# Kernel tuning notes

Measured on AMD Instinct MI355X. Metric: run time of the kernel, lower is better.

Reference implementation:

```python
import jax, jax.numpy as jnp
import numpy as np

HIDDEN = 4096
N_HEADS = 32
N_KV = 32
HEAD_DIM = 128
T = 2048
EPS = 1e-5
ROPE_THETA = 1000000.0


def rms_norm(x, w, eps=EPS):
    var = jnp.mean(x * x, axis=-1, keepdims=True)
    return x * jax.lax.rsqrt(var + eps) * w


def apply_rope(x, positions):
    # x: [T, H, D] ; neox-style (rotate halves), full rotary_dim = HEAD_DIM
    half = HEAD_DIM // 2
    inv_freq = 1.0 / (ROPE_THETA ** (jnp.arange(0, half, dtype=jnp.float32) / half))
    ang = positions.astype(jnp.float32)[:, None] * inv_freq  # [T, half]
    cos = jnp.cos(ang)[:, None, :]  # [T, 1, half]
    sin = jnp.sin(ang)[:, None, :]
    x1, x2 = x[..., :half], x[..., half:]
    return jnp.concatenate([x1 * cos - x2 * sin, x2 * cos + x1 * sin], axis=-1)


def setup_inputs() -> dict:
    key = jax.random.key(0)
    ks = jax.random.split(key, 5)
    s = 0.02
    qkv_out = (N_HEADS + 2 * N_KV) * HEAD_DIM
    return {
        "hidden_states": jax.random.normal(ks[0], (T, HIDDEN), jnp.float32),
        "positions": jnp.arange(T, dtype=jnp.int32),
        "w_qkv": jax.random.normal(ks[1], (qkv_out, HIDDEN), jnp.float32) * s,
        "b_qkv": jax.random.normal(ks[2], (qkv_out,), jnp.float32) * s,
        "q_norm_w": jnp.ones((N_HEADS * HEAD_DIM,), jnp.float32),
        "k_norm_w": jnp.ones((N_KV * HEAD_DIM,), jnp.float32),
        "w_o": jax.random.normal(ks[3], (HIDDEN, N_HEADS * HEAD_DIM), jnp.float32) * s,
    }


def reference(hidden_states, positions, w_qkv, b_qkv, q_norm_w, k_norm_w, w_o):
    q_size = N_HEADS * HEAD_DIM
    kv_size = N_KV * HEAD_DIM
    qkv = hidden_states @ w_qkv.T + b_qkv  # [T, q+2kv]
    q, k, v = jnp.split(qkv, [q_size, q_size + kv_size], axis=-1)
    # QK RMSNorm over the full flattened q / k widths (as in Molmo)
    q = rms_norm(q, q_norm_w)
    k = rms_norm(k, k_norm_w)
    q = apply_rope(q.reshape(T, N_HEADS, HEAD_DIM), positions)
    k = apply_rope(k.reshape(T, N_KV, HEAD_DIM), positions)
    v = v.reshape(T, N_KV, HEAD_DIM)
    scale = HEAD_DIM ** -0.5
    scores = jnp.einsum("qhd,khd->hqk", q, k) * scale  # [H, T, T]
    causal = positions[:, None] >= positions[None, :]
    scores = jnp.where(causal[None], scores, jnp.float32(-1e30))
    probs = jax.nn.softmax(scores, axis=-1)
    attn = jnp.einsum("hqk,khd->qhd", probs, v).reshape(T, N_HEADS * HEAD_DIM)
    return attn @ w_o.T
```

## Files before the change

kernel.cpp:

```cpp
#include <hip/hip_runtime.h>
#include <hip/hip_bf16.h>

#define T_SEQ 2048
#define NH 32
#define HD 128
#define QKV_N 12288
#define V_OFF 8192

typedef __bf16 bf16;
typedef __attribute__((ext_vector_type(8))) __bf16 bf16x8;
typedef __attribute__((ext_vector_type(4))) float f32x4;

#define GLDS16(g, l)                                                        \
  __builtin_amdgcn_global_load_lds(                                         \
      (const __attribute__((address_space(1))) void*)(g),                   \
      (__attribute__((address_space(3))) void*)(l), 16, 0, 0)

__device__ inline bf16x8 load8(const bf16* p) { return *(const bf16x8*)p; }
__device__ inline bf16x8 load8(const float* p) {
    f32x4 a = *(const f32x4*)p;
    f32x4 b = *(const f32x4*)(p + 4);
    bf16x8 r;
    r[0] = (bf16)a[0]; r[1] = (bf16)a[1]; r[2] = (bf16)a[2]; r[3] = (bf16)a[3];
    r[4] = (bf16)b[0]; r[5] = (bf16)b[1]; r[6] = (bf16)b[2]; r[7] = (bf16)b[3];
    return r;
}

__global__ __launch_bounds__(256)
void f32_to_bf16(const float* __restrict__ in, bf16* __restrict__ out, int n8)
{
    for (int i = blockIdx.x * 256 + threadIdx.x; i < n8; i += gridDim.x * 256)
        *(bf16x8*)(out + (size_t)i * 8) = load8(in + (size_t)i * 8);
}

#define BM 128
#define BN 128
#define BK 32

template <typename TO>
__global__ __launch_bounds__(256, 2)
void gemm_bt_glds(const bf16* __restrict__ A, int lda,
                  const bf16* __restrict__ B,
                  const float* __restrict__ bias,
                  TO* __restrict__ C, int ldc,
                  int mTiles, int colPerXcd, int K)
{
    __shared__ bf16 sA[BM * BK];
    __shared__ bf16 sB[BN * BK];
    const int tid  = threadIdx.x;
    const int wave = tid >> 6, lane = tid & 63;
    const int quad = lane >> 4, l16 = lane & 15;
    const int wm = wave >> 1, wn = wave & 1;

    int b = blockIdx.x;
    int xcd = b & 7, i = b >> 3;
    const int rowBase = (i % mTiles) * BM;
    const int colBase = (xcd * colPerXcd + i / mTiles) * BN;

    f32x4 acc[4][4] = {};

    for (int k0 = 0; k0 < K; k0 += BK) {
        __syncthreads();
        for (int r = 0; r < 2; ++r) {
            int cb = wave * 128 + r * 64;
            int c  = cb + lane;
            int row = c >> 2, kg = c & 3;
            GLDS16(A + (size_t)(rowBase + row) * lda + k0 + kg * 8, sA + cb * 8);
            GLDS16(B + (size_t)(colBase + row) * K + k0 + kg * 8, sB + cb * 8);
        }
        __syncthreads();

        bf16x8 af[4], bfr[4];
        for (int mi = 0; mi < 4; ++mi)
            af[mi] = *(const bf16x8*)(sA + (wm * 64 + mi * 16 + l16) * BK + quad * 8);
        for (int ni = 0; ni < 4; ++ni)
            bfr[ni] = *(const bf16x8*)(sB + (wn * 64 + ni * 16 + l16) * BK + quad * 8);
        for (int mi = 0; mi < 4; ++mi)
            for (int ni = 0; ni < 4; ++ni)
                acc[mi][ni] = __builtin_amdgcn_mfma_f32_16x16x32_bf16(
                    af[mi], bfr[ni], acc[mi][ni], 0, 0, 0);
    }

    for (int ni = 0; ni < 4; ++ni) {
        int col = colBase + wn * 64 + ni * 16 + l16;
        float bv = bias ? bias[col] : 0.0f;
        for (int mi = 0; mi < 4; ++mi) {
            int row0 = rowBase + wm * 64 + mi * 16 + quad * 4;
            for (int r = 0; r < 4; ++r)
                C[(size_t)(row0 + r) * ldc + col] = (TO)(acc[mi][ni][r] + bv);
        }
    }
}

template <typename TA, typename TB, typename TO>
__global__ __launch_bounds__(256, 2)
void gemm_bt_bias(const TA* __restrict__ A, int lda,
                  const TB* __restrict__ B,
                  const float* __restrict__ bias,
                  TO* __restrict__ C, int ldc,
                  int M, int N, int K)
{
    __shared__ bf16 sA[BM * BK];
    __shared__ bf16 sB[BN * BK];
    const int tid  = threadIdx.x;
    const int wave = tid >> 6, lane = tid & 63;
    const int quad = lane >> 4, l16 = lane & 15;
    const int wm = wave >> 1, wn = wave & 1;
    const int rowBase = blockIdx.x * BM;
    const int colBase = blockIdx.y * BN;

    int c0 = wave * 128 + lane;
    int rowA0 = c0 >> 2, kgA0 = c0 & 3;
    int rowA1 = (c0 + 64) >> 2, kgA1 = (c0 + 64) & 3;

    f32x4 acc[4][4] = {};

    for (int k0 = 0; k0 < K; k0 += BK) {
        bf16x8 ra0 = load8(A + (size_t)(rowBase + rowA0) * lda + k0 + kgA0 * 8);
        bf16x8 ra1 = load8(A + (size_t)(rowBase + rowA1) * lda + k0 + kgA1 * 8);
        bf16x8 rb0 = load8(B + (size_t)(colBase + rowA0) * K + k0 + kgA0 * 8);
        bf16x8 rb1 = load8(B + (size_t)(colBase + rowA1) * K + k0 + kgA1 * 8);
        __syncthreads();
        *(bf16x8*)(sA + rowA0 * BK + kgA0 * 8) = ra0;
        *(bf16x8*)(sA + rowA1 * BK + kgA1 * 8) = ra1;
        *(bf16x8*)(sB + rowA0 * BK + kgA0 * 8) = rb0;
        *(bf16x8*)(sB + rowA1 * BK + kgA1 * 8) = rb1;
        __syncthreads();

        bf16x8 af[4], bfr[4];
        for (int mi = 0; mi < 4; ++mi)
            af[mi] = *(const bf16x8*)(sA + (wm * 64 + mi * 16 + l16) * BK + quad * 8);
        for (int ni = 0; ni < 4; ++ni)
            bfr[ni] = *(const bf16x8*)(sB + (wn * 64 + ni * 16 + l16) * BK + quad * 8);
        for (int mi = 0; mi < 4; ++mi)
            for (int ni = 0; ni < 4; ++ni)
                acc[mi][ni] = __builtin_amdgcn_mfma_f32_16x16x32_bf16(
                    af[mi], bfr[ni], acc[mi][ni], 0, 0, 0);
    }

    for (int ni = 0; ni < 4; ++ni) {
        int col = colBase + wn * 64 + ni * 16 + l16;
        float bv = bias ? bias[col] : 0.0f;
        for (int mi = 0; mi < 4; ++mi) {
            int row0 = rowBase + wm * 64 + mi * 16 + quad * 4;
            for (int r = 0; r < 4; ++r)
                C[(size_t)(row0 + r) * ldc + col] = (TO)(acc[mi][ni][r] + bv);
        }
    }
}

__global__ __launch_bounds__(256)
void rmsnorm_rope(bf16* __restrict__ qkv, const float* __restrict__ qw,
                  const float* __restrict__ kw, const int* __restrict__ pos)
{
    const int t   = blockIdx.x;
    const int sel = blockIdx.y;
    bf16* x = qkv + (size_t)t * QKV_N + sel * 4096;
    const float* w = sel ? kw : qw;
    const int tid = threadIdx.x;

    float ss = 0.f;
    {
        int i0 = tid * 16;
        bf16x8 a = *(const bf16x8*)(x + i0);
        bf16x8 b = *(const bf16x8*)(x + i0 + 8);
        for (int j = 0; j < 8; ++j) { float fa = (float)a[j]; ss += fa * fa; }
        for (int j = 0; j < 8; ++j) { float fb = (float)b[j]; ss += fb * fb; }
    }
    for (int off = 1; off < 64; off <<= 1) ss += __shfl_xor(ss, off, 64);
    __shared__ float red[4];
    if ((tid & 63) == 0) red[tid >> 6] = ss;
    __syncthreads();
    float tot = red[0] + red[1] + red[2] + red[3];
    float rstd = rsqrtf(tot * (1.0f / 4096.0f) + 1e-5f);

    float fp = (float)pos[t];
    for (int i = tid; i < 2048; i += 256) {
        int h = i >> 6;
        int d = i & 63;
        int base = h * 128 + d;
        float x1 = (float)x[base]      * rstd * w[base];
        float x2 = (float)x[base + 64] * rstd * w[base + 64];
        float ang = fp * exp2f(-(float)d * 0.31143075889569023f);
        float s, c;
        sincosf(ang, &s, &c);
        x[base]      = (bf16)(x1 * c - x2 * s);
        x[base + 64] = (bf16)(x2 * c + x1 * s);
    }
}

__global__ __launch_bounds__(256)
void v_transpose(const bf16* __restrict__ qkv, bf16* __restrict__ vt)
{
    __shared__ bf16 tile[64][65];
    int t0 = blockIdx.x * 64, d0 = blockIdx.y * 64, h = blockIdx.z;
    int x = threadIdx.x & 63, y4 = threadIdx.x >> 6;
    for (int yy = y4; yy < 64; yy += 4)
        tile[yy][x] = qkv[(size_t)(t0 + yy) * QKV_N + V_OFF + h * HD + d0 + x];
    __syncthreads();
    for (int yy = y4; yy < 64; yy += 4)
        vt[(size_t)(h * HD + d0 + yy) * T_SEQ + t0 + x] = tile[x][yy];
}

#define SKP 136
#define SVP 72
#define PBP 72

__global__ __launch_bounds__(256, 2)
void flash_attn(bf16* qkv, const bf16* vt)
{
    __shared__ bf16 sK[64 * SKP];
    __shared__ bf16 sV[128 * SVP];
    __shared__ bf16 pbuf[4 * 16 * PBP];

    const int tid  = threadIdx.x;
    const int wave = tid >> 6, lane = tid & 63;
    const int quad = lane >> 4, l16 = lane & 15;
    const int h    = blockIdx.y;
    const int blk  = blockIdx.x;
    const int q0w  = blk * 64 + wave * 16;

    bf16x8 qf[4];
    {
        const bf16* qrow = qkv + (size_t)(q0w + l16) * QKV_N + h * HD;
        for (int c = 0; c < 4; ++c)
            qf[c] = *(const bf16x8*)(qrow + c * 32 + quad * 8);
    }

    f32x4 oacc[8] = {};
    float m2[4], l[4];
    for (int r = 0; r < 4; ++r) { m2[r] = -1e30f; l[r] = 0.f; }

    const float sc = 0.08838834764831845f * 1.4426950408889634f;
    bf16* pb = pbuf + wave * 16 * PBP;
    const int rowa = q0w + quad * 4;
    const int kend = blk * 64;

    for (int kb = 0; kb <= kend; kb += 64) {
        __syncthreads();
        for (int j = 0; j < 4; ++j) {
            int c = tid + j * 256;
            int r = c >> 4, off = (c & 15) * 8;
            bf16x8 v = *(const bf16x8*)(qkv + (size_t)(kb + r) * QKV_N + 4096 + h * HD + off);
            *(bf16x8*)(sK + r * SKP + off) = v;
        }
        for (int j = 0; j < 4; ++j) {
            int c = tid + j * 256;
            int d = c >> 3, off = (c & 7) * 8;
            bf16x8 v = *(const bf16x8*)(vt + (size_t)(h * HD + d) * T_SEQ + kb + off);
            *(bf16x8*)(sV + d * SVP + off) = v;
        }
        __syncthreads();

        const bool diag = (kb == kend);
        const int stmax = diag ? (wave + 1) : 4;

        f32x4 s[4] = {};
        for (int st = 0; st < 4; ++st) {
            if (st >= stmax) break;
            const bf16* kbase = sK + (st * 16 + l16) * SKP + quad * 8;
            for (int c = 0; c < 4; ++c) {
                bf16x8 kf = *(const bf16x8*)(kbase + c * 32);
                s[st] = __builtin_amdgcn_mfma_f32_16x16x32_bf16(qf[c], kf, s[st], 0, 0, 0);
            }
        }
        for (int st = 0; st < 4; ++st) {
            int col = kb + st * 16 + l16;
            for (int r = 0; r < 4; ++r) {
                float v = s[st][r] * sc;
                s[st][r] = (col <= rowa + r) ? v : -1e30f;
            }
        }
        float alpha[4];
        for (int r = 0; r < 4; ++r) {
            float mx = fmaxf(fmaxf(s[0][r], s[1][r]), fmaxf(s[2][r], s[3][r]));
            for (int off = 1; off < 16; off <<= 1)
                mx = fmaxf(mx, __shfl_xor(mx, off, 64));
            float mnew = fmaxf(m2[r], mx);
            alpha[r] = exp2f(m2[r] - mnew);
            float ps = 0.f;
            for (int st = 0; st < 4; ++st) {
                float p = exp2f(s[st][r] - mnew);
                s[st][r] = p;
                ps += p;
            }
            for (int off = 1; off < 16; off <<= 1)
                ps += __shfl_xor(ps, off, 64);
            l[r] = l[r] * alpha[r] + ps;
            m2[r] = mnew;
        }
        for (int c = 0; c < 8; ++c)
            for (int r = 0; r < 4; ++r)
                oacc[c][r] *= alpha[r];
        for (int st = 0; st < 4; ++st)
            for (int r = 0; r < 4; ++r)
                pb[(quad * 4 + r) * PBP + st * 16 + l16] = (bf16)s[st][r];
        __builtin_amdgcn_s_waitcnt(0xC07F);
        for (int ph = 0; ph < 2; ++ph) {
            bf16x8 pf = *(const bf16x8*)(pb + l16 * PBP + ph * 32 + quad * 8);
            for (int c = 0; c < 8; ++c) {
                bf16x8 vf = *(const bf16x8*)(sV + (c * 16 + l16) * SVP + ph * 32 + quad * 8);
                oacc[c] = __builtin_amdgcn_mfma_f32_16x16x32_bf16(pf, vf, oacc[c], 0, 0, 0);
            }
        }
    }

    for (int r = 0; r < 4; ++r) {
        float inv = 1.0f / l[r];
        int t = q0w + quad * 4 + r;
        for (int c = 0; c < 8; ++c)
            qkv[(size_t)t * QKV_N + V_OFF + h * HD + c * 16 + l16] =
                (bf16)(oacc[c][r] * inv);
    }
}

extern "C" void kernel_launch(void* const* d_in, const int* in_sizes, int n_in,
                              void* d_out, int out_size, void* d_ws, size_t ws_size,
                              hipStream_t stream)
{
    const float* hidden   = (const float*)d_in[0];
    const int*   pos      = (const int*)d_in[1];
    const float* w_qkv    = (const float*)d_in[2];
    const float* b_qkv    = (const float*)d_in[3];
    const float* q_norm_w = (const float*)d_in[4];
    const float* k_norm_w = (const float*)d_in[5];
    const float* w_o      = (const float*)d_in[6];
    float* out = (float*)d_out;

    bf16* qkv = (bf16*)d_ws;
    bf16* vt  = qkv + (size_t)T_SEQ * QKV_N;
    bf16* wqb = vt  + (size_t)4096 * T_SEQ;
    bf16* wob = wqb + (size_t)QKV_N * 4096;
    bf16* hib = wob + (size_t)4096 * 4096;
    const size_t need = ((size_t)T_SEQ * QKV_N + (size_t)4096 * T_SEQ +
                         (size_t)QKV_N * 4096 + (size_t)4096 * 4096 +
                         (size_t)T_SEQ * 4096) * 2;

    if (ws_size >= need) {
        f32_to_bf16<<<2048, 256, 0, stream>>>(hidden, hib, T_SEQ * 4096 / 8);
        f32_to_bf16<<<8192, 256, 0, stream>>>(w_qkv, wqb, QKV_N * 4096 / 8);
        f32_to_bf16<<<4096, 256, 0, stream>>>(w_o, wob, 4096 * 4096 / 8);

        gemm_bt_glds<bf16><<<8 * 16 * 12, 256, 0, stream>>>(
            hib, 4096, wqb, b_qkv, qkv, QKV_N, 16, 12, 4096);
        rmsnorm_rope<<<dim3(T_SEQ, 2), 256, 0, stream>>>(qkv, q_norm_w, k_norm_w, pos);
        v_transpose<<<dim3(T_SEQ / 64, 2, NH), 256, 0, stream>>>(qkv, vt);
        flash_attn<<<dim3(T_SEQ / 64, NH), 256, 0, stream>>>(qkv, vt);
        gemm_bt_glds<float><<<8 * 16 * 4, 256, 0, stream>>>(
            qkv + V_OFF, QKV_N, wob, nullptr, out, 4096, 16, 4, 4096);
    } else {
        gemm_bt_bias<float, float, bf16><<<dim3(T_SEQ / BM, QKV_N / BN), 256, 0, stream>>>(
            hidden, 4096, w_qkv, b_qkv, qkv, QKV_N, T_SEQ, QKV_N, 4096);
        rmsnorm_rope<<<dim3(T_SEQ, 2), 256, 0, stream>>>(qkv, q_norm_w, k_norm_w, pos);
        v_transpose<<<dim3(T_SEQ / 64, 2, NH), 256, 0, stream>>>(qkv, vt);
        flash_attn<<<dim3(T_SEQ / 64, NH), 256, 0, stream>>>(qkv, vt);
        gemm_bt_bias<bf16, float, float><<<dim3(T_SEQ / BM, 4096 / BN), 256, 0, stream>>>(
            qkv + V_OFF, QKV_N, w_o, nullptr, out, 4096, T_SEQ, 4096, 4096);
    }
}
```

Baseline: 960.4 us.

## Pair causal query blocks per workgroup and transpose QK^T MFMA layout

Each flash-attention workgroup now handles two query blocks, blk and 31-blk, so every workgroup does about the same amount of causal work and the grid halves. The S = K·Q^T MFMA operand order is swapped so each lane owns a single query row. Row max and sum then need only two cross-quad shuffles instead of per-row 16-lane butterflies, and the alpha and l values are redistributed with __shfl for the PV accumulation. P is written to LDS as bf16x4 vectors instead of scalar stores. The grid shrinks to 512 workgroups, which may reduce occupancy on a 256-CU device.

```diff
diff --git a/kernel.cpp b/kernel.cpp
--- a/kernel.cpp
+++ b/kernel.cpp
@@ -8,6 +8,7 @@
 #define V_OFF 8192
 
 typedef __bf16 bf16;
+typedef __attribute__((ext_vector_type(4))) __bf16 bf16x4;
 typedef __attribute__((ext_vector_type(8))) __bf16 bf16x8;
 typedef __attribute__((ext_vector_type(4))) float f32x4;
 
@@ -217,100 +218,108 @@
     const int wave = tid >> 6, lane = tid & 63;
     const int quad = lane >> 4, l16 = lane & 15;
     const int h    = blockIdx.y;
-    const int blk  = blockIdx.x;
-    const int q0w  = blk * 64 + wave * 16;
-
-    bf16x8 qf[4];
-    {
-        const bf16* qrow = qkv + (size_t)(q0w + l16) * QKV_N + h * HD;
-        for (int c = 0; c < 4; ++c)
-            qf[c] = *(const bf16x8*)(qrow + c * 32 + quad * 8);
-    }
-
-    f32x4 oacc[8] = {};
-    float m2[4], l[4];
-    for (int r = 0; r < 4; ++r) { m2[r] = -1e30f; l[r] = 0.f; }
 
     const float sc = 0.08838834764831845f * 1.4426950408889634f;
     bf16* pb = pbuf + wave * 16 * PBP;
-    const int rowa = q0w + quad * 4;
-    const int kend = blk * 64;
-
-    for (int kb = 0; kb <= kend; kb += 64) {
-        __syncthreads();
-        for (int j = 0; j < 4; ++j) {
-            int c = tid + j * 256;
-            int r = c >> 4, off = (c & 15) * 8;
-            bf16x8 v = *(const bf16x8*)(qkv + (size_t)(kb + r) * QKV_N + 4096 + h * HD + off);
-            *(bf16x8*)(sK + r * SKP + off) = v;
-        }
-        for (int j = 0; j < 4; ++j) {
-            int c = tid + j * 256;
-            int d = c >> 3, off = (c & 7) * 8;
-            bf16x8 v = *(const bf16x8*)(vt + (size_t)(h * HD + d) * T_SEQ + kb + off);
-            *(bf16x8*)(sV + d * SVP + off) = v;
-        }
-        __syncthreads();
-
-        const bool diag = (kb == kend);
-        const int stmax = diag ? (wave + 1) : 4;
-
-        f32x4 s[4] = {};
-        for (int st = 0; st < 4; ++st) {
-            if (st >= stmax) break;
-            const bf16* kbase = sK + (st * 16 + l16) * SKP + quad * 8;
-            for (int c = 0; c < 4; ++c) {
-                bf16x8 kf = *(const bf16x8*)(kbase + c * 32);
-                s[st] = __builtin_amdgcn_mfma_f32_16x16x32_bf16(qf[c], kf, s[st], 0, 0, 0);
-            }
-        }
-        for (int st = 0; st < 4; ++st) {
-            int col = kb + st * 16 + l16;
-            for (int r = 0; r < 4; ++r) {
-                float v = s[st][r] * sc;
-                s[st][r] = (col <= rowa + r) ? v : -1e30f;
-            }
-        }
-        float alpha[4];
+
+    for (int half = 0; half < 2; ++half) {
+        const int blk  = half ? (31 - (int)blockIdx.x) : (int)blockIdx.x;
+        const int q0w  = blk * 64 + wave * 16;
+        const int kend = blk * 64;
+        const int qln  = q0w + l16;
+
+        bf16x8 qf[4];
+        {
+            const bf16* qrow = qkv + (size_t)qln * QKV_N + h * HD;
+            for (int c = 0; c < 4; ++c)
+                qf[c] = *(const bf16x8*)(qrow + c * 32 + quad * 8);
+        }
+
+        f32x4 oacc[8] = {};
+        float m2 = -1e30f, lsum = 0.f;
+
+        for (int kb = 0; kb <= kend; kb += 64) {
+            __syncthreads();
+            for (int j = 0; j < 4; ++j) {
+                int c = tid + j * 256;
+                int r = c >> 4, off = (c & 15) * 8;
+                bf16x8 v = *(const bf16x8*)(qkv + (size_t)(kb + r) * QKV_N + 4096 + h * HD + off);
+                *(bf16x8*)(sK + r * SKP + off) = v;
+            }
+            for (int j = 0; j < 4; ++j) {
+                int c = tid + j * 256;
+                int d = c >> 3, off = (c & 7) * 8;
+                bf16x8 v = *(const bf16x8*)(vt + (size_t)(h * HD + d) * T_SEQ + kb + off);
+                *(bf16x8*)(sV + d * SVP + off) = v;
+            }
+            __syncthreads();
+
+            const int stmax = (kb == kend) ? (wave + 1) : 4;
+
+            f32x4 s[4] = {};
+            for (int st = 0; st < 4; ++st) {
+                if (st >= stmax) break;
+                const bf16* kbase = sK + (st * 16 + l16) * SKP + quad * 8;
+                for (int c = 0; c < 4; ++c) {
+                    bf16x8 kf = *(const bf16x8*)(kbase + c * 32);
+                    s[st] = __builtin_amdgcn_mfma_f32_16x16x32_bf16(kf, qf[c], s[st], 0, 0, 0);
+                }
+            }
+            for (int st = 0; st < 4; ++st) {
+                int k0r = kb + st * 16 + quad * 4;
+                for (int r = 0; r < 4; ++r) {
+                    float v = s[st][r] * sc;
+                    s[st][r] = (k0r + r <= qln) ? v : -1e30f;
+                }
+            }
+            float mx = -1e30f;
+            for (int st = 0; st < 4; ++st)
+                for (int r = 0; r < 4; ++r) mx = fmaxf(mx, s[st][r]);
+            mx = fmaxf(mx, __shfl_xor(mx, 16, 64));
+            mx = fmaxf(mx, __shfl_xor(mx, 32, 64));
+            float mnew  = fmaxf(m2, mx);
+            float alpha = exp2f(m2 - mnew);
+            float ps = 0.f;
+            for (int st = 0; st < 4; ++st)
+                for (int r = 0; r < 4; ++r) {
+                    float p = exp2f(s[st][r] - mnew);
+                    s[st][r] = p;
+                    ps += p;
+                }
+            ps += __shfl_xor(ps, 16, 64);
+            ps += __shfl_xor(ps, 32, 64);
+            lsum = lsum * alpha + ps;
+            m2 = mnew;
+
+            float ar[4];
+            for (int r = 0; r < 4; ++r) ar[r] = __shfl(alpha, quad * 4 + r, 64);
+            for (int c = 0; c < 8; ++c)
+                for (int r = 0; r < 4; ++r) oacc[c][r] *= ar[r];
+
+            for (int st = 0; st < 4; ++st) {
+                bf16x4 pw;
+                for (int r = 0; r < 4; ++r) pw[r] = (bf16)s[st][r];
+                *(bf16x4*)(pb + l16 * PBP + st * 16 + quad * 4) = pw;
+            }
+            __builtin_amdgcn_s_waitcnt(0xC07F);
+            for (int ph = 0; ph < 2; ++ph) {
+                bf16x8 pf = *(const bf16x8*)(pb + l16 * PBP + ph * 32 + quad * 8);
+                for (int c = 0; c < 8; ++c) {
+                    bf16x8 vf = *(const bf16x8*)(sV + (c * 16 + l16) * SVP + ph * 32 + quad * 8);
+                    oacc[c] = __builtin_amdgcn_mfma_f32_16x16x32_bf16(pf, vf, oacc[c], 0, 0, 0);
+                }
+            }
+        }
+
+        float lr[4];
+        for (int r = 0; r < 4; ++r) lr[r] = __shfl(lsum, quad * 4 + r, 64);
         for (int r = 0; r < 4; ++r) {
-            float mx = fmaxf(fmaxf(s[0][r], s[1][r]), fmaxf(s[2][r], s[3][r]));
-            for (int off = 1; off < 16; off <<= 1)
-                mx = fmaxf(mx, __shfl_xor(mx, off, 64));
-            float mnew = fmaxf(m2[r], mx);
-            alpha[r] = exp2f(m2[r] - mnew);
-            float ps = 0.f;
-            for (int st = 0; st < 4; ++st) {
-                float p = exp2f(s[st][r] - mnew);
-                s[st][r] = p;
-                ps += p;
-            }
-            for (int off = 1; off < 16; off <<= 1)
-                ps += __shfl_xor(ps, off, 64);
-            l[r] = l[r] * alpha[r] + ps;
-            m2[r] = mnew;
-        }
-        for (int c = 0; c < 8; ++c)
-            for (int r = 0; r < 4; ++r)
-                oacc[c][r] *= alpha[r];
-        for (int st = 0; st < 4; ++st)
-            for (int r = 0; r < 4; ++r)
-                pb[(quad * 4 + r) * PBP + st * 16 + l16] = (bf16)s[st][r];
-        __builtin_amdgcn_s_waitcnt(0xC07F);
-        for (int ph = 0; ph < 2; ++ph) {
-            bf16x8 pf = *(const bf16x8*)(pb + l16 * PBP + ph * 32 + quad * 8);
-            for (int c = 0; c < 8; ++c) {
-                bf16x8 vf = *(const bf16x8*)(sV + (c * 16 + l16) * SVP + ph * 32 + quad * 8);
-                oacc[c] = __builtin_amdgcn_mfma_f32_16x16x32_bf16(pf, vf, oacc[c], 0, 0, 0);
-            }
-        }
-    }
-
-    for (int r = 0; r < 4; ++r) {
-        float inv = 1.0f / l[r];
-        int t = q0w + quad * 4 + r;
-        for (int c = 0; c < 8; ++c)
-            qkv[(size_t)t * QKV_N + V_OFF + h * HD + c * 16 + l16] =
-                (bf16)(oacc[c][r] * inv);
+            float inv = 1.0f / lr[r];
+            int t = q0w + quad * 4 + r;
+            for (int c = 0; c < 8; ++c)
+                qkv[(size_t)t * QKV_N + V_OFF + h * HD + c * 16 + l16] =
+                    (bf16)(oacc[c][r] * inv);
+        }
     }
 }
 
@@ -345,7 +354,7 @@
             hib, 4096, wqb, b_qkv, qkv, QKV_N, 16, 12, 4096);
         rmsnorm_rope<<<dim3(T_SEQ, 2), 256, 0, stream>>>(qkv, q_norm_w, k_norm_w, pos);
         v_transpose<<<dim3(T_SEQ / 64, 2, NH), 256, 0, stream>>>(qkv, vt);
-        flash_attn<<<dim3(T_SEQ / 64, NH), 256, 0, stream>>>(qkv, vt);
+        flash_attn<<<dim3(T_SEQ / 128, NH), 256, 0, stream>>>(qkv, vt);
         gemm_bt_glds<float><<<8 * 16 * 4, 256, 0, stream>>>(
             qkv + V_OFF, QKV_N, wob, nullptr, out, 4096, 16, 4, 4096);
     } else {
@@ -353,7 +362,7 @@
             hidden, 4096, w_qkv, b_qkv, qkv, QKV_N, T_SEQ, QKV_N, 4096);
         rmsnorm_rope<<<dim3(T_SEQ, 2), 256, 0, stream>>>(qkv, q_norm_w, k_norm_w, pos);
         v_transpose<<<dim3(T_SEQ / 64, 2, NH), 256, 0, stream>>>(qkv, vt);
-        flash_attn<<<dim3(T_SEQ / 64, NH), 256, 0, stream>>>(qkv, vt);
+        flash_attn<<<dim3(T_SEQ / 128, NH), 256, 0, stream>>>(qkv, vt);
         gemm_bt_bias<bf16, float, float><<<dim3(T_SEQ / BM, 4096 / BN), 256, 0, stream>>>(
             qkv + V_OFF, QKV_N, w_o, nullptr, out, 4096, T_SEQ, 4096, 4096);
     }
```

New measurement: 846.6 us. 11.8% less time.
